# Performance work log

Hardware: AMD Instinct MI355X
Metric: run time of the kernel (lower is better)

Reference implementation:

```python
import jax, jax.numpy as jnp
import numpy as np

T = 65536   # total tokens across all packed sequences
C = 768     # channels
K = 5       # kernel_size (odd)
NSEQ = 16   # number of packed sequences (>1 -> masked varlen path)


def setup_inputs() -> dict:
    key = jax.random.key(0)
    k1, k2, k3, k4 = jax.random.split(key, 4)
    x = jax.random.normal(k1, (T, C), dtype=jnp.float32)
    # cu_seqlens: [0, sorted interior boundaries, T]
    interior = jnp.sort(jax.random.randint(k2, (NSEQ - 1,), 1, T)).astype(jnp.int32)
    cu_seqlens = jnp.concatenate([
        jnp.zeros((1,), dtype=jnp.int32),
        interior,
        jnp.full((1,), T, dtype=jnp.int32),
    ])
    # depthwise conv weight [C, K] (== conv.weight[:, 0, :]) and bias [C]
    weight = jax.random.normal(k3, (C, K), dtype=jnp.float32) * 0.1
    bias = jax.random.normal(k4, (C,), dtype=jnp.float32) * 0.01
    return {"x": x, "cu_seqlens": cu_seqlens, "weight": weight, "bias": bias}


def reference(x, cu_seqlens, weight, bias):
    # Varlen Canon depthwise mixing with sequence-boundary masking.
    # x: [T, C] float32; cu_seqlens: [n_seqs+1] int32; weight: [C, K]; bias: [C].
    t = x.shape[0]
    radius = weight.shape[1] // 2
    positions = jnp.arange(t, dtype=cu_seqlens.dtype)
    # seq_id[i] = which packed sequence token i belongs to
    seq_id = jnp.searchsorted(cu_seqlens[1:], positions, side='right')
    out = jnp.zeros_like(x)
    for k, offset in enumerate(range(-radius, radius + 1)):  # K taps (small fixed loop)
        rolled_x = jnp.roll(x, -offset, axis=0)
        rolled_id = jnp.roll(seq_id, -offset, axis=0)
        valid = (rolled_id == seq_id)[:, None]               # [T, 1] boundary mask
        out = out + jnp.where(valid, rolled_x, 0.0) * weight[:, k]
    out = out + bias
    return x + out  # residual add
```

## Files before the change

kernel.cpp:

```cpp
#include <hip/hip_runtime.h>


#define CC  768
#define C4V (CC / 4)
#define KK  5
#define RR  2
#define TPB 16

__global__ __launch_bounds__(C4V) void canon_dwconv_kernel(
    const float4* __restrict__ x4,
    const int*    __restrict__ cu,
    int nseq,
    const float*  __restrict__ weight,
    const float4* __restrict__ bias4,
    float4*       __restrict__ out4,
    int T)
{
    const int c4 = threadIdx.x;
    const int t0 = (int)blockIdx.x * TPB;
    const int c  = c4 * 4;

    float w[KK][4];
#pragma unroll
    for (int j = 0; j < 4; ++j)
#pragma unroll
        for (int k = 0; k < KK; ++k)
            w[k][j] = weight[(c + j) * KK + k];

    const float4 b = bias4[c4];

    float4 win[KK];
#pragma unroll
    for (int i = 0; i < KK - 1; ++i) {
        int r  = t0 - RR + i;
        int rc = min(max(r, 0), T - 1);
        win[i] = x4[(size_t)rc * C4V + c4];
    }

    int sid = 0;
    while (sid < nseq && cu[sid + 1] <= t0) ++sid;

#pragma unroll
    for (int tt = 0; tt < TPB; ++tt) {
        const int t = t0 + tt;
        if (t < T) {
            {
                int rc = min(t + RR, T - 1);
                win[(tt + KK - 1) % KK] = x4[(size_t)rc * C4V + c4];
            }
            while (sid < nseq && cu[sid + 1] <= t) ++sid;
            const int start = cu[sid];
            const int end   = cu[sid + 1];

            const float4 r0 = win[(tt + 0) % KK];
            const float4 r1 = win[(tt + 1) % KK];
            const float4 r2 = win[(tt + 2) % KK];
            const float4 r3 = win[(tt + 3) % KK];
            const float4 r4 = win[(tt + 4) % KK];

            const float m0 = (t - 2 >= start) ? 1.0f : 0.0f;
            const float m1 = (t - 1 >= start) ? 1.0f : 0.0f;
            const float m3 = (t + 1 <  end)  ? 1.0f : 0.0f;
            const float m4 = (t + 2 <  end)  ? 1.0f : 0.0f;

            float4 o;
            o.x = r2.x + b.x + r2.x * w[2][0]
                + r0.x * (w[0][0] * m0) + r1.x * (w[1][0] * m1)
                + r3.x * (w[3][0] * m3) + r4.x * (w[4][0] * m4);
            o.y = r2.y + b.y + r2.y * w[2][1]
                + r0.y * (w[0][1] * m0) + r1.y * (w[1][1] * m1)
                + r3.y * (w[3][1] * m3) + r4.y * (w[4][1] * m4);
            o.z = r2.z + b.z + r2.z * w[2][2]
                + r0.z * (w[0][2] * m0) + r1.z * (w[1][2] * m1)
                + r3.z * (w[3][2] * m3) + r4.z * (w[4][2] * m4);
            o.w = r2.w + b.w + r2.w * w[2][3]
                + r0.w * (w[0][3] * m0) + r1.w * (w[1][3] * m1)
                + r3.w * (w[3][3] * m3) + r4.w * (w[4][3] * m4);

            out4[(size_t)t * C4V + c4] = o;
        }
    }
}

extern "C" void kernel_launch(void* const* d_in, const int* in_sizes, int n_in,
                              void* d_out, int out_size, void* d_ws, size_t ws_size,
                              hipStream_t stream) {
    const float4* x4     = (const float4*)d_in[0];
    const int*    cu     = (const int*)d_in[1];
    const float*  weight = (const float*)d_in[2];
    const float4* bias4  = (const float4*)d_in[3];
    float4*       out4   = (float4*)d_out;

    const int T    = in_sizes[0] / CC;
    const int nseq = in_sizes[1] - 1;

    const int grid = (T + TPB - 1) / TPB;
    canon_dwconv_kernel<<<grid, C4V, 0, stream>>>(x4, cu, nseq, weight, bias4, out4, T);
}
```

Baseline: 345.8 us.

## Add interior fast path without masks, double tokens per block, nontemporal stores

Blocks whose token range, including the halo, lies entirely inside one sequence now take a fast path with no clamping, no per-token boundary search and no masks. TPB rises from 16 to 32, which cuts the redundant halo loads per block and halves the grid size. Output stores become nontemporal to reduce cache pollution. The cost is more code, higher register pressure from the larger unroll, and fewer blocks in flight.

```diff
diff --git a/kernel.cpp b/kernel.cpp
--- a/kernel.cpp
+++ b/kernel.cpp
@@ -5,15 +5,17 @@
 #define C4V (CC / 4)
 #define KK  5
 #define RR  2
-#define TPB 16
+#define TPB 32
+
+typedef float v4f __attribute__((ext_vector_type(4)));
 
 __global__ __launch_bounds__(C4V) void canon_dwconv_kernel(
-    const float4* __restrict__ x4,
-    const int*    __restrict__ cu,
+    const v4f* __restrict__ x4,
+    const int* __restrict__ cu,
     int nseq,
-    const float*  __restrict__ weight,
-    const float4* __restrict__ bias4,
-    float4*       __restrict__ out4,
+    const float* __restrict__ weight,
+    const v4f* __restrict__ bias4,
+    v4f* __restrict__ out4,
     int T)
 {
     const int c4 = threadIdx.x;
@@ -27,57 +29,80 @@
         for (int k = 0; k < KK; ++k)
             w[k][j] = weight[(c + j) * KK + k];
 
-    const float4 b = bias4[c4];
-
-    float4 win[KK];
-#pragma unroll
-    for (int i = 0; i < KK - 1; ++i) {
-        int r  = t0 - RR + i;
-        int rc = min(max(r, 0), T - 1);
-        win[i] = x4[(size_t)rc * C4V + c4];
-    }
+    const v4f b = bias4[c4];
 
     int sid = 0;
     while (sid < nseq && cu[sid + 1] <= t0) ++sid;
+    const int start0 = cu[sid];
+    const int end0   = cu[sid + 1];
+
+    const bool interior = (start0 <= t0 - RR) && (end0 >= t0 + TPB + RR);
+
+    v4f win[KK];
+
+    if (interior) {
+#pragma unroll
+        for (int i = 0; i < KK - 1; ++i)
+            win[i] = x4[(size_t)(t0 - RR + i) * C4V + c4];
 
 #pragma unroll
-    for (int tt = 0; tt < TPB; ++tt) {
-        const int t = t0 + tt;
-        if (t < T) {
-            {
+        for (int tt = 0; tt < TPB; ++tt) {
+            const int t = t0 + tt;
+            win[(tt + KK - 1) % KK] = x4[(size_t)(t + RR) * C4V + c4];
+
+            const v4f r0 = win[(tt + 0) % KK];
+            const v4f r1 = win[(tt + 1) % KK];
+            const v4f r2 = win[(tt + 2) % KK];
+            const v4f r3 = win[(tt + 3) % KK];
+            const v4f r4 = win[(tt + 4) % KK];
+
+            v4f o;
+#pragma unroll
+            for (int j = 0; j < 4; ++j)
+                o[j] = r2[j] + b[j] + r0[j] * w[0][j] + r1[j] * w[1][j]
+                     + r2[j] * w[2][j] + r3[j] * w[3][j] + r4[j] * w[4][j];
+
+            __builtin_nontemporal_store(o, &out4[(size_t)t * C4V + c4]);
+        }
+    } else {
+#pragma unroll
+        for (int i = 0; i < KK - 1; ++i) {
+            int r  = t0 - RR + i;
+            int rc = min(max(r, 0), T - 1);
+            win[i] = x4[(size_t)rc * C4V + c4];
+        }
+
+#pragma unroll
+        for (int tt = 0; tt < TPB; ++tt) {
+            const int t = t0 + tt;
+            if (t < T) {
                 int rc = min(t + RR, T - 1);
                 win[(tt + KK - 1) % KK] = x4[(size_t)rc * C4V + c4];
+
+                while (sid < nseq && cu[sid + 1] <= t) ++sid;
+                const int start = cu[sid];
+                const int end   = cu[sid + 1];
+
+                const v4f r0 = win[(tt + 0) % KK];
+                const v4f r1 = win[(tt + 1) % KK];
+                const v4f r2 = win[(tt + 2) % KK];
+                const v4f r3 = win[(tt + 3) % KK];
+                const v4f r4 = win[(tt + 4) % KK];
+
+                const float m0 = (t - 2 >= start) ? 1.0f : 0.0f;
+                const float m1 = (t - 1 >= start) ? 1.0f : 0.0f;
+                const float m3 = (t + 1 <  end)  ? 1.0f : 0.0f;
+                const float m4 = (t + 2 <  end)  ? 1.0f : 0.0f;
+
+                v4f o;
+#pragma unroll
+                for (int j = 0; j < 4; ++j)
+                    o[j] = r2[j] + b[j] + r2[j] * w[2][j]
+                         + r0[j] * (w[0][j] * m0) + r1[j] * (w[1][j] * m1)
+                         + r3[j] * (w[3][j] * m3) + r4[j] * (w[4][j] * m4);
+
+                __builtin_nontemporal_store(o, &out4[(size_t)t * C4V + c4]);
             }
-            while (sid < nseq && cu[sid + 1] <= t) ++sid;
-            const int start = cu[sid];
-            const int end   = cu[sid + 1];
-
-            const float4 r0 = win[(tt + 0) % KK];
-            const float4 r1 = win[(tt + 1) % KK];
-            const float4 r2 = win[(tt + 2) % KK];
-            const float4 r3 = win[(tt + 3) % KK];
-            const float4 r4 = win[(tt + 4) % KK];
-
-            const float m0 = (t - 2 >= start) ? 1.0f : 0.0f;
-            const float m1 = (t - 1 >= start) ? 1.0f : 0.0f;
-            const float m3 = (t + 1 <  end)  ? 1.0f : 0.0f;
-            const float m4 = (t + 2 <  end)  ? 1.0f : 0.0f;
-
-            float4 o;
-            o.x = r2.x + b.x + r2.x * w[2][0]
-                + r0.x * (w[0][0] * m0) + r1.x * (w[1][0] * m1)
-                + r3.x * (w[3][0] * m3) + r4.x * (w[4][0] * m4);
-            o.y = r2.y + b.y + r2.y * w[2][1]
-                + r0.y * (w[0][1] * m0) + r1.y * (w[1][1] * m1)
-                + r3.y * (w[3][1] * m3) + r4.y * (w[4][1] * m4);
-            o.z = r2.z + b.z + r2.z * w[2][2]
-                + r0.z * (w[0][2] * m0) + r1.z * (w[1][2] * m1)
-                + r3.z * (w[3][2] * m3) + r4.z * (w[4][2] * m4);
-            o.w = r2.w + b.w + r2.w * w[2][3]
-                + r0.w * (w[0][3] * m0) + r1.w * (w[1][3] * m1)
-                + r3.w * (w[3][3] * m3) + r4.w * (w[4][3] * m4);
-
-            out4[(size_t)t * C4V + c4] = o;
         }
     }
 }
@@ -85,11 +110,11 @@
 extern "C" void kernel_launch(void* const* d_in, const int* in_sizes, int n_in,
                               void* d_out, int out_size, void* d_ws, size_t ws_size,
                               hipStream_t stream) {
-    const float4* x4     = (const float4*)d_in[0];
-    const int*    cu     = (const int*)d_in[1];
-    const float*  weight = (const float*)d_in[2];
-    const float4* bias4  = (const float4*)d_in[3];
-    float4*       out4   = (float4*)d_out;
+    const v4f*   x4     = (const v4f*)d_in[0];
+    const int*   cu     = (const int*)d_in[1];
+    const float* weight = (const float*)d_in[2];
+    const v4f*   bias4  = (const v4f*)d_in[3];
+    v4f*         out4   = (v4f*)d_out;
 
     const int T    = in_sizes[0] / CC;
     const int nseq = in_sizes[1] - 1;
```

Measured after the change: 355.8 us. +2.9%, slower.
